# Kernel optimization log

Measured on AMD Instinct MI355X. Metric: run time of the kernel, lower is better.

Reference implementation:

```python
import jax, jax.numpy as jnp
import numpy as np

BLOCK = 128
SPARSE_BLOCK = 128
SF = 4
NEG = jnp.finfo(jnp.float32).min


def _unfold(x, size, step):
    # x: (..., T, d) -> (..., b, size, d) overlapping windows (torch unfold + transpose)
    b = (x.shape[-2] - size) // step + 1
    idx = np.arange(b)[:, None] * step + np.arange(size)
    return x[..., idx, :]


def _pad_tokens(x, s, pad_value):
    cfg = [(0, 0)] * (x.ndim - 2) + [(s, s), (0, 0)]
    return jnp.pad(x, cfg, constant_values=pad_value)


def _local_blocks(x, pad_value):
    size, step = BLOCK * 3, BLOCK
    s = (size - step) // 2
    return _unfold(_pad_tokens(x, s, pad_value), size, step)


def _sparse_blocks(x, pad_value):
    size0, step = SPARSE_BLOCK * 3, BLOCK // SF
    odd = step % 2
    size = size0 * 2
    s = (size - step) // 2 + odd
    xw = _unfold(_pad_tokens(x, s, pad_value), size, step)
    if odd:
        xw = xw[..., :-1, :, :]
    u = (size - BLOCK * 3 // SF) // 2 + odd
    sb = SPARSE_BLOCK
    u_ = u + odd
    return jnp.concatenate([xw[..., u - sb:u, :], xw[..., -u_:-u_ + sb, :]], axis=-2)


def _cat_gsl(x_global, x_sparse, x_local):
    # x_local: (n,h,b,t_loc,d); broadcast global over block axis
    b = x_local.shape[-3]
    g = jnp.broadcast_to(x_global[..., None, :, :],
                         x_global.shape[:-2] + (b,) + x_global.shape[-2:])
    return jnp.concatenate([g, x_sparse, x_local], axis=-2)


def _build_lsg(x, x_sparse, x_global, pad_value):
    loc = _local_blocks(x, pad_value)
    sp = _sparse_blocks(x_sparse, pad_value)
    return _cat_gsl(x_global, sp, loc)


def reference(query_layer, key_layer, value_layer, attention_mask,
              sparse_key, sparse_value, sparse_mask,
              global_key, global_value, global_mask):
    n, h, t, d = query_layer.shape
    n_blocks = t // BLOCK

    keys = _build_lsg(key_layer, sparse_key, global_key, 0.0)      # (n,h,b,K,d)
    vals = _build_lsg(value_layer, sparse_value, global_value, 0.0)

    # masks: (n,1,1,T) treated as d=1 token data after transpose
    m = jnp.swapaxes(attention_mask, -1, -2)    # (n,1,t,1)
    sm = jnp.swapaxes(sparse_mask, -1, -2)      # (n,1,t/SF,1)
    gm = jnp.swapaxes(global_mask, -1, -2)      # (n,1,g,1)
    mask = _build_lsg(m, sm, gm, NEG)           # (n,1,b,K,1)
    mask = jnp.swapaxes(mask, -1, -2)           # (n,1,b,1,K)

    q = query_layer.reshape(n, h, n_blocks, BLOCK, d)
    scores = jnp.einsum('nhbqd,nhbkd->nhbqk', q, keys) / jnp.sqrt(jnp.float32(d))
    probs = jax.nn.softmax(scores + mask, axis=-1)
    ctx = jnp.einsum('nhbqk,nhbkd->nhbqd', probs, vals)
    return ctx.reshape(n, h, t, d)


def setup_inputs() -> dict:
    key = jax.random.key(0)
    n, h, t, d = 2, 12, 4096, 64
    g = 64
    ts = t // SF
    k = jax.random.split(key, 7)
    return {
        'query_layer': jax.random.normal(k[0], (n, h, t, d), jnp.float32),
        'key_layer': jax.random.normal(k[1], (n, h, t, d), jnp.float32),
        'value_layer': jax.random.normal(k[2], (n, h, t, d), jnp.float32),
        'attention_mask': jnp.zeros((n, 1, 1, t), jnp.float32),
        'sparse_key': jax.random.normal(k[3], (n, h, ts, d), jnp.float32),
        'sparse_value': jax.random.normal(k[4], (n, h, ts, d), jnp.float32),
        'sparse_mask': jnp.zeros((n, 1, 1, ts), jnp.float32),
        'global_key': jax.random.normal(k[5], (n, h, g, d), jnp.float32),
        'global_value': jax.random.normal(k[6], (n, h, g, d), jnp.float32),
        'global_mask': jnp.zeros((n, 1, 1, g), jnp.float32),
    }
```

## Files before the change

kernel.cpp:

```cpp
#include <hip/hip_runtime.h>
#include <hip/hip_bf16.h>

typedef __attribute__((ext_vector_type(8))) short short8;
typedef __attribute__((ext_vector_type(4))) float f32x4;

#define LOG2E 1.44269504f
#define SCL2  0.18033688f
#define MNEG  -3.0e38f
#define MINIT -1.0e30f

__device__ __forceinline__ short f2bf(float f) {
  union { float f; unsigned u; } x; x.f = f;
  return (short)((x.u + 0x7FFFu + ((x.u >> 16) & 1u)) >> 16);
}
__device__ __forceinline__ float exp2g(float x) {
  float r; asm("v_exp_f32 %0, %1" : "=v"(r) : "v"(x)); return r;
}
__device__ __forceinline__ unsigned cvt_pk_bf16(float lo, float hi) {
  unsigned r;
  asm("v_cvt_pk_bf16_f32 %0, %1, %2" : "=v"(r) : "v"(lo), "v"(hi));
  return r;
}

__device__ __forceinline__ void conv_one(
    const float* __restrict__ src, short* __restrict__ dst,
    int Tin, int pad, int cid) {
  int Tpad = Tin + 2 * pad;
  int row = cid >> 3;
  int d0 = (cid & 7) * 8;
  int tok = row % Tpad;
  int nh = row / Tpad;
  int st = tok - pad;
  short8 o;
  if (st >= 0 && st < Tin) {
    const float4* sp = (const float4*)(src + ((size_t)nh * Tin + st) * 64 + d0);
    float4 f0 = sp[0], f1 = sp[1];
    o[0] = f2bf(f0.x); o[1] = f2bf(f0.y); o[2] = f2bf(f0.z); o[3] = f2bf(f0.w);
    o[4] = f2bf(f1.x); o[5] = f2bf(f1.y); o[6] = f2bf(f1.z); o[7] = f2bf(f1.w);
  } else {
#pragma unroll
    for (int j = 0; j < 8; ++j) o[j] = 0;
  }
  *(short8*)(dst + (size_t)row * 64 + d0) = o;
}

__global__ __launch_bounds__(256) void conv_fused(
    const float* __restrict__ K, const float* __restrict__ SK,
    const float* __restrict__ GK,
    short* __restrict__ KL, short* __restrict__ KS, short* __restrict__ KG,
    const float* __restrict__ am, const float* __restrict__ sm,
    const float* __restrict__ gm,
    float* __restrict__ AM2, float* __restrict__ SM2, float* __restrict__ GM2) {
  int cid = blockIdx.x * 256 + threadIdx.x;
  const int nL = 24 * 4352 * 8;
  const int nS = nL + 24 * 1344 * 8;
  const int nG = nS + 24 * 64 * 8;
  if (cid < nL) { conv_one(K, KL, 4096, 128, cid); return; }
  if (cid < nS) { conv_one(SK, KS, 1024, 160, cid - nL); return; }
  if (cid < nG) { conv_one(GK, KG, 64, 0, cid - nS); return; }
  int i = cid - nG;
  if (i < 2 * 4352) {
    int n = i / 4352, rr = i % 4352, s = rr - 128;
    AM2[i] = (s >= 0 && s < 4096) ? am[n * 4096 + s] * LOG2E : MNEG;
  } else if (i < 2 * 4352 + 2 * 1344) {
    int j = i - 2 * 4352;
    int n = j / 1344, rr = j % 1344, s = rr - 160;
    SM2[j] = (s >= 0 && s < 1024) ? sm[n * 1024 + s] * LOG2E : MNEG;
  } else if (i < 2 * 4352 + 2 * 1344 + 2 * 64) {
    int j = i - 2 * 4352 - 2 * 1344;
    GM2[j] = gm[j] * LOG2E;
  }
}

__device__ __forceinline__ void transv_one(
    const float* __restrict__ src, short* __restrict__ dst,
    int Tin, int pad, int tiles, int bidx, int tid, short (*lt)[72]) {
  int tile = bidx % tiles;
  int nh = bidx / tiles;
  int Tpad = Tin + 2 * pad;
  int c0 = tile * 64;
  int tok = tid >> 2;
  int dc = (tid & 3) * 16;
  int st = c0 + tok - pad;
  if (st >= 0 && st < Tin) {
    const float4* sp = (const float4*)(src + ((size_t)nh * Tin + st) * 64 + dc);
#pragma unroll
    for (int i = 0; i < 4; ++i) {
      float4 f = sp[i];
      lt[tok][dc + i * 4 + 0] = f2bf(f.x);
      lt[tok][dc + i * 4 + 1] = f2bf(f.y);
      lt[tok][dc + i * 4 + 2] = f2bf(f.z);
      lt[tok][dc + i * 4 + 3] = f2bf(f.w);
    }
  } else {
#pragma unroll
    for (int i = 0; i < 16; ++i) lt[tok][dc + i] = 0;
  }
  __syncthreads();
  int d = tid >> 2;
  int tc = (tid & 3) * 16;
  short8 o0, o1;
#pragma unroll
  for (int j = 0; j < 8; ++j) { o0[j] = lt[tc + j][d]; o1[j] = lt[tc + 8 + j][d]; }
  short* dp = dst + ((size_t)nh * 64 + d) * Tpad + c0 + tc;
  *(short8*)(dp) = o0;
  *(short8*)(dp + 8) = o1;
}

__global__ __launch_bounds__(256) void transv_fused(
    const float* __restrict__ V, const float* __restrict__ SV,
    const float* __restrict__ GV,
    short* __restrict__ VTL, short* __restrict__ VTS, short* __restrict__ VTG) {
  __shared__ short lt[64][72];
  int bidx = blockIdx.x;
  int tid = threadIdx.x;
  if (bidx < 24 * 68) { transv_one(V, VTL, 4096, 128, 68, bidx, tid, lt); return; }
  bidx -= 24 * 68;
  if (bidx < 24 * 21) { transv_one(SV, VTS, 1024, 160, 21, bidx, tid, lt); return; }
  bidx -= 24 * 21;
  transv_one(GV, VTG, 64, 0, 1, bidx, tid, lt);
}

__global__ __launch_bounds__(512, 4) void lsg_attn5(
    const short* __restrict__ KL, const short* __restrict__ VTL,
    const short* __restrict__ KS, const short* __restrict__ VTS,
    const short* __restrict__ KG, const short* __restrict__ VTG,
    const float* __restrict__ AM2, const float* __restrict__ SM2,
    const float* __restrict__ GM2,
    const float* __restrict__ q_, float* __restrict__ out) {
  constexpr int TPL = 4352, TPS = 1344;
  __shared__ __align__(16) char smem[49152];

  int bid = blockIdx.x;
  bid = (bid & 7) * 96 + (bid >> 3);
  const int b = bid & 31, nh = bid >> 5, n_ = nh / 12;
  const int tid = threadIdx.x;
  const int wid = tid >> 6, lane = tid & 63;
  const int c = lane & 15, g = lane >> 4;
  const int r = tid >> 3, ch = tid & 7;
  const int skey = 4 * (r & 15) + (r >> 4);
  char* pbase = smem + 32768 + wid * 2048;
  const unsigned stg = ((unsigned)r << 7) + ((unsigned)(ch * 16) ^ ((unsigned)(r & 7) << 4));

  const float* qb = q_ + ((size_t)nh * 4096 + (size_t)b * 128 + wid * 16) * 64;
  short8 qa[2];
#pragma unroll
  for (int kc = 0; kc < 2; ++kc) {
    const float* qp = qb + (size_t)c * 64 + kc * 32 + g * 8;
    float4 f0 = *(const float4*)(qp);
    float4 f1 = *(const float4*)(qp + 4);
    short8 tq;
    tq[0] = f2bf(f0.x); tq[1] = f2bf(f0.y); tq[2] = f2bf(f0.z); tq[3] = f2bf(f0.w);
    tq[4] = f2bf(f1.x); tq[5] = f2bf(f1.y); tq[6] = f2bf(f1.z); tq[7] = f2bf(f1.w);
    qa[kc] = tq;
  }

  f32x4 acc[4];
  float mrun[4], lrun[4];
#pragma unroll
  for (int dd = 0; dd < 4; ++dd) acc[dd] = f32x4{0.f, 0.f, 0.f, 0.f};
#pragma unroll
  for (int j = 0; j < 4; ++j) { mrun[j] = MINIT; lrun[j] = 0.f; }

  auto src_for = [&](int t, const short*& kp, const short*& vp,
                     const float*& mp, int& stride) {
    if (t == 0) {
      kp = KG + (size_t)nh * (64 * 64);
      vp = VTG + (size_t)nh * (64 * 64);
      mp = GM2 + n_ * 64;
      stride = 64;
    } else if (t <= 4) {
      int r0 = b * 32 + (t - 1) * 64 + (t >= 3 ? 96 : 0);
      kp = KS + ((size_t)nh * TPS + r0) * 64;
      vp = VTS + (size_t)nh * (64 * TPS) + r0;
      mp = SM2 + n_ * TPS + r0;
      stride = TPS;
    } else {
      int r0 = b * 128 + (t - 5) * 64;
      kp = KL + ((size_t)nh * TPL + r0) * 64;
      vp = VTL + (size_t)nh * (64 * TPL) + r0;
      mp = AM2 + n_ * TPL + r0;
      stride = TPL;
    }
  };

  short8 kr, vr;
  float m_cur[4], m_nxt[4];

  {
    const short* kp; const short* vp; const float* mp; int st;
    src_for(0, kp, vp, mp, st);
    kr = *(const short8*)(kp + skey * 64 + ch * 8);
    vr = *(const short8*)(vp + (size_t)r * st + ch * 8);
#pragma unroll
    for (int i = 0; i < 4; ++i) m_cur[i] = mp[4 * c + i];
    *(short8*)(smem + stg) = kr;
    *(short8*)(smem + 16384 + stg) = vr;
    src_for(1, kp, vp, mp, st);
    kr = *(const short8*)(kp + skey * 64 + ch * 8);
    vr = *(const short8*)(vp + (size_t)r * st + ch * 8);
  }

  for (int t = 0; t < 11; ++t) {
    asm volatile("s_waitcnt lgkmcnt(0)\n\ts_barrier" ::: "memory");
    const int cur = t & 1, nxt = cur ^ 1;
    char* kbuf = smem + cur * 8192;
    char* vbuf = smem + 16384 + cur * 8192;

    short8 bk[4][2];
#pragma unroll
    for (int kt = 0; kt < 4; ++kt)
#pragma unroll
      for (int kc = 0; kc < 2; ++kc) {
        unsigned off = ((unsigned)(kt * 16 + c) << 7) +
                       ((unsigned)(kc * 64 + g * 16) ^ ((unsigned)(c & 7) << 4));
        bk[kt][kc] = *(const short8*)(kbuf + off);
      }

    if (t < 10) {
      *(short8*)(smem + nxt * 8192 + stg) = kr;
      *(short8*)(smem + 16384 + nxt * 8192 + stg) = vr;
    }
    if (t < 9) {
      const short* kp; const short* vp; const float* mp; int st;
      src_for(t + 2, kp, vp, mp, st);
      kr = *(const short8*)(kp + skey * 64 + ch * 8);
      vr = *(const short8*)(vp + (size_t)r * st + ch * 8);
    }
    if (t < 10) {
      const short* kp; const short* vp; const float* mp; int st;
      src_for(t + 1, kp, vp, mp, st);
#pragma unroll
      for (int i = 0; i < 4; ++i) m_nxt[i] = mp[4 * c + i];
    }

    f32x4 s4[4];
    __builtin_amdgcn_s_setprio(1);
#pragma unroll
    for (int kt = 0; kt < 4; ++kt) {
      f32x4 z = f32x4{0.f, 0.f, 0.f, 0.f};
      z = __builtin_amdgcn_mfma_f32_16x16x32_bf16(qa[0], bk[kt][0], z, 0, 0, 0);
      z = __builtin_amdgcn_mfma_f32_16x16x32_bf16(qa[1], bk[kt][1], z, 0, 0, 0);
      s4[kt] = z;
    }
    __builtin_amdgcn_s_setprio(0);
#pragma unroll
    for (int kt = 0; kt < 4; ++kt)
#pragma unroll
      for (int j = 0; j < 4; ++j)
        s4[kt][j] = fmaf(s4[kt][j], SCL2, m_cur[kt]);

    float rs[4];
    float worst = 0.f;
#pragma unroll
    for (int j = 0; j < 4; ++j) {
      float mo = mrun[j];
      float p0 = exp2g(s4[0][j] - mo);
      float p1 = exp2g(s4[1][j] - mo);
      float p2 = exp2g(s4[2][j] - mo);
      float p3 = exp2g(s4[3][j] - mo);
      rs[j] = (p0 + p1) + (p2 + p3);
      worst = fmaxf(worst, rs[j]);
      unsigned w0 = cvt_pk_bf16(p0, p1);
      unsigned w1 = cvt_pk_bf16(p2, p3);
      int row = 4 * g + j;
      unsigned bo = ((unsigned)row << 7) + ((unsigned)c << 3);
      bo ^= (unsigned)((row & 7) << 4);
      uint2 u; u.x = w0; u.y = w1;
      *(uint2*)(pbase + bo) = u;
    }

    if (__any(worst > 4096.f)) {
#pragma unroll
      for (int j = 0; j < 4; ++j) {
        float v0 = s4[0][j], v1 = s4[1][j];
        float v2 = s4[2][j], v3 = s4[3][j];
        float tv = fmaxf(fmaxf(v0, v1), fmaxf(v2, v3));
        tv = fmaxf(tv, __shfl_xor(tv, 1));
        tv = fmaxf(tv, __shfl_xor(tv, 2));
        tv = fmaxf(tv, __shfl_xor(tv, 4));
        tv = fmaxf(tv, __shfl_xor(tv, 8));
        float mo = mrun[j];
        float mn = fmaxf(mo, tv);
        float sc = exp2g(mo - mn);
#pragma unroll
        for (int dd = 0; dd < 4; ++dd) acc[dd][j] *= sc;
        float p0 = exp2g(v0 - mn), p1 = exp2g(v1 - mn);
        float p2 = exp2g(v2 - mn), p3 = exp2g(v3 - mn);
        lrun[j] = lrun[j] * sc + ((p0 + p1) + (p2 + p3));
        mrun[j] = mn;
        unsigned w0 = cvt_pk_bf16(p0, p1);
        unsigned w1 = cvt_pk_bf16(p2, p3);
        int row = 4 * g + j;
        unsigned bo = ((unsigned)row << 7) + ((unsigned)c << 3);
        bo ^= (unsigned)((row & 7) << 4);
        uint2 u; u.x = w0; u.y = w1;
        *(uint2*)(pbase + bo) = u;
      }
    } else {
#pragma unroll
      for (int j = 0; j < 4; ++j) lrun[j] += rs[j];
    }

#pragma unroll
    for (int kk = 0; kk < 2; ++kk) {
      unsigned bo = ((unsigned)c << 7) + (unsigned)(kk * 64 + g * 16);
      bo ^= (unsigned)((c & 7) << 4);
      short8 pa = *(const short8*)(pbase + bo);
      __builtin_amdgcn_s_setprio(1);
#pragma unroll
      for (int dd = 0; dd < 4; ++dd) {
        unsigned voff = ((unsigned)(dd * 16 + c) << 7) +
                        ((unsigned)(kk * 64 + g * 16) ^ ((unsigned)(c & 7) << 4));
        short8 bv = *(const short8*)(vbuf + voff);
        acc[dd] = __builtin_amdgcn_mfma_f32_16x16x32_bf16(pa, bv, acc[dd], 0, 0, 0);
      }
      __builtin_amdgcn_s_setprio(0);
    }
#pragma unroll
    for (int i = 0; i < 4; ++i) m_cur[i] = m_nxt[i];
  }

  float inv[4];
#pragma unroll
  for (int j = 0; j < 4; ++j) {
    float l = lrun[j];
    l += __shfl_xor(l, 1);
    l += __shfl_xor(l, 2);
    l += __shfl_xor(l, 4);
    l += __shfl_xor(l, 8);
    inv[j] = 1.f / l;
  }
  __syncthreads();
  float* fst = (float*)smem + wid * (16 * 68);
#pragma unroll
  for (int j = 0; j < 4; ++j)
#pragma unroll
    for (int dd = 0; dd < 4; ++dd)
      fst[(4 * g + j) * 68 + dd * 16 + c] = acc[dd][j] * inv[j];
  int rr = lane >> 2, cc = lane & 3;
  const float* fs = (float*)smem + wid * (16 * 68) + rr * 68 + cc * 16;
  float* op = out + ((size_t)nh * 4096 + (size_t)b * 128 + wid * 16 + rr) * 64 + cc * 16;
#pragma unroll
  for (int i = 0; i < 4; ++i)
    *(float4*)(op + i * 4) = *(const float4*)(fs + i * 4);
}

__global__ __launch_bounds__(256) void lsg_attn_fb(
    const float* __restrict__ q_,  const float* __restrict__ k_,
    const float* __restrict__ v_,  const float* __restrict__ amask,
    const float* __restrict__ sk,  const float* __restrict__ sv,
    const float* __restrict__ smk, const float* __restrict__ gk,
    const float* __restrict__ gv,  const float* __restrict__ gmk,
    float* __restrict__ out) {
  constexpr int T = 4096, D = 64, TS = 1024;
  constexpr float NEGF = -3.402823466e38f;
  __shared__ __align__(16) short k_lds[32][72];
  __shared__ __align__(16) short v_lds[64][40];
  __shared__ __align__(16) short p_lds[4][32][40];
  __shared__ float m_lds[32];
  const int bid = blockIdx.x;
  const int b = bid & 31, nh = bid >> 5, n_ = nh / 12;
  const int tid = threadIdx.x, wid = tid >> 6, lane = tid & 63;
  const int c = lane & 15, g = lane >> 4;
  const float* qb = q_ + ((size_t)nh * T + (size_t)b * 128) * D;
  const float* kb = k_ + (size_t)nh * T * D;
  const float* vb = v_ + (size_t)nh * T * D;
  const float* skb = sk + (size_t)nh * TS * D;
  const float* svb = sv + (size_t)nh * TS * D;
  const float* gkb = gk + (size_t)nh * 64 * D;
  const float* gvb = gv + (size_t)nh * 64 * D;
  const float* am = amask + (size_t)n_ * T;
  const float* sm = smk + (size_t)n_ * TS;
  const float* gm = gmk + (size_t)n_ * 64;
  short8 qa[2][2];
#pragma unroll
  for (int mt = 0; mt < 2; ++mt)
#pragma unroll
    for (int kc = 0; kc < 2; ++kc) {
      const float* qp = qb + (size_t)(wid * 32 + mt * 16 + c) * D + kc * 32 + g * 8;
      short8 t;
#pragma unroll
      for (int j = 0; j < 8; ++j) t[j] = f2bf(qp[j]);
      qa[mt][kc] = t;
    }
  f32x4 acc[2][4];
#pragma unroll
  for (int mt = 0; mt < 2; ++mt)
#pragma unroll
    for (int dd = 0; dd < 4; ++dd) acc[mt][dd] = f32x4{0.f, 0.f, 0.f, 0.f};
  float mrun[2][4], lrun[2][4];
#pragma unroll
  for (int mt = 0; mt < 2; ++mt)
#pragma unroll
    for (int j = 0; j < 4; ++j) { mrun[mt][j] = NEGF; lrun[mt][j] = 0.f; }
  const int key_local = tid >> 3;
  const int seg = tid & 7;
  const int d0 = seg * 8;
  for (int tile = 0; tile < 22; ++tile) {
    __syncthreads();
    {
      const int kk = tile * 32 + key_local;
      const float* ksrc; const float* vsrc; float mval; bool valid;
      if (kk < 64) {
        ksrc = gkb + kk * D; vsrc = gvb + kk * D; mval = gm[kk]; valid = true;
      } else if (kk < 320) {
        int s = b * 32 - 160 + (kk - 64) + ((kk >= 192) ? 96 : 0);
        valid = (s >= 0) && (s < TS);
        int sc2 = valid ? s : 0;
        ksrc = skb + sc2 * D; vsrc = svb + sc2 * D;
        mval = valid ? sm[sc2] : NEGF;
      } else {
        int tt = b * 128 - 128 + (kk - 320);
        valid = (tt >= 0) && (tt < T);
        int tc = valid ? tt : 0;
        ksrc = kb + tc * D; vsrc = vb + tc * D;
        mval = valid ? am[tc] : NEGF;
      }
      short8 k8; short v8[8];
      if (valid) {
#pragma unroll
        for (int j = 0; j < 8; ++j) { k8[j] = f2bf(ksrc[d0 + j]); v8[j] = f2bf(vsrc[d0 + j]); }
      } else {
#pragma unroll
        for (int j = 0; j < 8; ++j) { k8[j] = 0; v8[j] = 0; }
      }
      *(short8*)(&k_lds[key_local][d0]) = k8;
#pragma unroll
      for (int j = 0; j < 8; ++j) v_lds[d0 + j][key_local] = v8[j];
      if (seg == 0) m_lds[key_local] = mval;
    }
    __syncthreads();
    short8 bk[2][2];
#pragma unroll
    for (int kt = 0; kt < 2; ++kt)
#pragma unroll
      for (int kc = 0; kc < 2; ++kc)
        bk[kt][kc] = *(const short8*)(&k_lds[kt * 16 + c][kc * 32 + g * 8]);
    f32x4 s_[2][2];
#pragma unroll
    for (int mt = 0; mt < 2; ++mt)
#pragma unroll
      for (int kt = 0; kt < 2; ++kt) {
        f32x4 z = f32x4{0.f, 0.f, 0.f, 0.f};
        z = __builtin_amdgcn_mfma_f32_16x16x32_bf16(qa[mt][0], bk[kt][0], z, 0, 0, 0);
        z = __builtin_amdgcn_mfma_f32_16x16x32_bf16(qa[mt][1], bk[kt][1], z, 0, 0, 0);
        s_[mt][kt] = z;
      }
    const float msk0 = m_lds[c];
    const float msk1 = m_lds[16 + c];
#pragma unroll
    for (int mt = 0; mt < 2; ++mt) {
#pragma unroll
      for (int j = 0; j < 4; ++j) {
        float s0 = s_[mt][0][j] * 0.125f + msk0;
        float s1 = s_[mt][1][j] * 0.125f + msk1;
        float tv = fmaxf(s0, s1);
        tv = fmaxf(tv, __shfl_xor(tv, 1));
        tv = fmaxf(tv, __shfl_xor(tv, 2));
        tv = fmaxf(tv, __shfl_xor(tv, 4));
        tv = fmaxf(tv, __shfl_xor(tv, 8));
        float mold = mrun[mt][j];
        float mnew = fmaxf(mold, tv);
        float scale = __expf(mold - mnew);
        mrun[mt][j] = mnew;
        float p0 = __expf(s0 - mnew);
        float p1 = __expf(s1 - mnew);
        lrun[mt][j] = lrun[mt][j] * scale + p0 + p1;
#pragma unroll
        for (int dd = 0; dd < 4; ++dd) acc[mt][dd][j] *= scale;
        p_lds[wid][mt * 16 + g * 4 + j][c] = f2bf(p0);
        p_lds[wid][mt * 16 + g * 4 + j][16 + c] = f2bf(p1);
      }
    }
    __syncthreads();
#pragma unroll
    for (int mt = 0; mt < 2; ++mt) {
      short8 pa = *(const short8*)(&p_lds[wid][mt * 16 + c][g * 8]);
#pragma unroll
      for (int dd = 0; dd < 4; ++dd) {
        short8 bv = *(const short8*)(&v_lds[dd * 16 + c][g * 8]);
        acc[mt][dd] = __builtin_amdgcn_mfma_f32_16x16x32_bf16(pa, bv, acc[mt][dd], 0, 0, 0);
      }
    }
  }
  float* ob = out + ((size_t)nh * T + (size_t)b * 128 + (size_t)wid * 32) * D;
#pragma unroll
  for (int mt = 0; mt < 2; ++mt)
#pragma unroll
    for (int j = 0; j < 4; ++j) {
      float l = lrun[mt][j];
      l += __shfl_xor(l, 1);
      l += __shfl_xor(l, 2);
      l += __shfl_xor(l, 4);
      l += __shfl_xor(l, 8);
      float inv = 1.f / l;
      int row = mt * 16 + g * 4 + j;
#pragma unroll
      for (int dd = 0; dd < 4; ++dd)
        ob[(size_t)row * D + dd * 16 + c] = acc[mt][dd][j] * inv;
    }
}

extern "C" void kernel_launch(void* const* d_in, const int* in_sizes, int n_in,
                              void* d_out, int out_size, void* d_ws, size_t ws_size,
                              hipStream_t stream) {
  const float* q  = (const float*)d_in[0];
  const float* k  = (const float*)d_in[1];
  const float* v  = (const float*)d_in[2];
  const float* am = (const float*)d_in[3];
  const float* sk = (const float*)d_in[4];
  const float* sv = (const float*)d_in[5];
  const float* sm = (const float*)d_in[6];
  const float* gk = (const float*)d_in[7];
  const float* gv = (const float*)d_in[8];
  const float* gm = (const float*)d_in[9];
  float* out = (float*)d_out;

  size_t off = 0;
  char* base = (char*)d_ws;
  auto alloc = [&](size_t bytes) { void* p = base + off; off += bytes; return p; };
  short* KL  = (short*)alloc(13369344);
  short* VTL = (short*)alloc(13369344);
  short* KS  = (short*)alloc(4128768);
  short* VTS = (short*)alloc(4128768);
  short* KG  = (short*)alloc(196608);
  short* VTG = (short*)alloc(196608);
  float* AM2 = (float*)alloc(34816);
  float* SM2 = (float*)alloc(10752);
  float* GM2 = (float*)alloc(512);

  if (off <= ws_size) {
    hipLaunchKernelGGL(conv_fused, dim3(4365), dim3(256), 0, stream,
                       k, sk, gk, KL, KS, KG, am, sm, gm, AM2, SM2, GM2);
    hipLaunchKernelGGL(transv_fused, dim3(2160), dim3(256), 0, stream,
                       v, sv, gv, VTL, VTS, VTG);
    hipLaunchKernelGGL(lsg_attn5, dim3(768), dim3(512), 0, stream,
                       KL, VTL, KS, VTS, KG, VTG, AM2, SM2, GM2, q, out);
  } else {
    hipLaunchKernelGGL(lsg_attn_fb, dim3(768), dim3(256), 0, stream,
                       q, k, v, am, sk, sv, sm, gk, gv, gm, out);
  }
}
```

Before: 59.52 us.

## Merge prepass kernels and skip fully padded key tiles per block

The K-conversion, V-transpose and mask prepasses are merged into one launch, which removes one kernel launch and its boundary. The attention kernel now builds a per-block list of key tiles and drops tiles that, for edge blocks, lie entirely in the padding region. Those tiles are fully masked, so edge blocks do less load and MFMA work. The tile index is now a runtime value, which may cost some unrolling and address-computation efficiency, and the merged prepass mixes block types that use shared memory differently.

```diff
diff --git a/kernel.cpp b/kernel.cpp
--- a/kernel.cpp
+++ b/kernel.cpp
@@ -44,34 +44,6 @@
   *(short8*)(dst + (size_t)row * 64 + d0) = o;
 }
 
-__global__ __launch_bounds__(256) void conv_fused(
-    const float* __restrict__ K, const float* __restrict__ SK,
-    const float* __restrict__ GK,
-    short* __restrict__ KL, short* __restrict__ KS, short* __restrict__ KG,
-    const float* __restrict__ am, const float* __restrict__ sm,
-    const float* __restrict__ gm,
-    float* __restrict__ AM2, float* __restrict__ SM2, float* __restrict__ GM2) {
-  int cid = blockIdx.x * 256 + threadIdx.x;
-  const int nL = 24 * 4352 * 8;
-  const int nS = nL + 24 * 1344 * 8;
-  const int nG = nS + 24 * 64 * 8;
-  if (cid < nL) { conv_one(K, KL, 4096, 128, cid); return; }
-  if (cid < nS) { conv_one(SK, KS, 1024, 160, cid - nL); return; }
-  if (cid < nG) { conv_one(GK, KG, 64, 0, cid - nS); return; }
-  int i = cid - nG;
-  if (i < 2 * 4352) {
-    int n = i / 4352, rr = i % 4352, s = rr - 128;
-    AM2[i] = (s >= 0 && s < 4096) ? am[n * 4096 + s] * LOG2E : MNEG;
-  } else if (i < 2 * 4352 + 2 * 1344) {
-    int j = i - 2 * 4352;
-    int n = j / 1344, rr = j % 1344, s = rr - 160;
-    SM2[j] = (s >= 0 && s < 1024) ? sm[n * 1024 + s] * LOG2E : MNEG;
-  } else if (i < 2 * 4352 + 2 * 1344 + 2 * 64) {
-    int j = i - 2 * 4352 - 2 * 1344;
-    GM2[j] = gm[j] * LOG2E;
-  }
-}
-
 __device__ __forceinline__ void transv_one(
     const float* __restrict__ src, short* __restrict__ dst,
     int Tin, int pad, int tiles, int bidx, int tid, short (*lt)[72]) {
@@ -107,21 +79,46 @@
   *(short8*)(dp + 8) = o1;
 }
 
-__global__ __launch_bounds__(256) void transv_fused(
+__global__ __launch_bounds__(256) void prepass_all(
+    const float* __restrict__ K, const float* __restrict__ SK,
+    const float* __restrict__ GK,
     const float* __restrict__ V, const float* __restrict__ SV,
     const float* __restrict__ GV,
-    short* __restrict__ VTL, short* __restrict__ VTS, short* __restrict__ VTG) {
+    short* __restrict__ KL, short* __restrict__ KS, short* __restrict__ KG,
+    short* __restrict__ VTL, short* __restrict__ VTS, short* __restrict__ VTG,
+    const float* __restrict__ am, const float* __restrict__ sm,
+    const float* __restrict__ gm,
+    float* __restrict__ AM2, float* __restrict__ SM2, float* __restrict__ GM2) {
   __shared__ short lt[64][72];
   int bidx = blockIdx.x;
   int tid = threadIdx.x;
-  if (bidx < 24 * 68) { transv_one(V, VTL, 4096, 128, 68, bidx, tid, lt); return; }
-  bidx -= 24 * 68;
-  if (bidx < 24 * 21) { transv_one(SV, VTS, 1024, 160, 21, bidx, tid, lt); return; }
-  bidx -= 24 * 21;
-  transv_one(GV, VTG, 64, 0, 1, bidx, tid, lt);
-}
-
-__global__ __launch_bounds__(512, 4) void lsg_attn5(
+  if (bidx < 3264) { conv_one(K,  KL, 4096, 128, bidx * 256 + tid); return; }
+  bidx -= 3264;
+  if (bidx < 1008) { conv_one(SK, KS, 1024, 160, bidx * 256 + tid); return; }
+  bidx -= 1008;
+  if (bidx < 48)   { conv_one(GK, KG, 64, 0, bidx * 256 + tid); return; }
+  bidx -= 48;
+  if (bidx < 1632) { transv_one(V,  VTL, 4096, 128, 68, bidx, tid, lt); return; }
+  bidx -= 1632;
+  if (bidx < 504)  { transv_one(SV, VTS, 1024, 160, 21, bidx, tid, lt); return; }
+  bidx -= 504;
+  if (bidx < 24)   { transv_one(GV, VTG, 64, 0, 1, bidx, tid, lt); return; }
+  bidx -= 24;
+  int i = bidx * 256 + tid;
+  if (i < 2 * 4352) {
+    int n = i / 4352, rr = i % 4352, s = rr - 128;
+    AM2[i] = (s >= 0 && s < 4096) ? am[n * 4096 + s] * LOG2E : MNEG;
+  } else if (i < 2 * 4352 + 2 * 1344) {
+    int j = i - 2 * 4352;
+    int n = j / 1344, rr = j % 1344, s = rr - 160;
+    SM2[j] = (s >= 0 && s < 1024) ? sm[n * 1024 + s] * LOG2E : MNEG;
+  } else {
+    int j = i - 2 * 4352 - 2 * 1344;
+    GM2[j] = gm[j] * LOG2E;
+  }
+}
+
+__global__ __launch_bounds__(512, 4) void lsg_attn8(
     const short* __restrict__ KL, const short* __restrict__ VTL,
     const short* __restrict__ KS, const short* __restrict__ VTS,
     const short* __restrict__ KG, const short* __restrict__ VTG,
@@ -141,6 +138,19 @@
   const int skey = 4 * (r & 15) + (r >> 4);
   char* pbase = smem + 32768 + wid * 2048;
   const unsigned stg = ((unsigned)r << 7) + ((unsigned)(ch * 16) ^ ((unsigned)(r & 7) << 4));
+
+  unsigned long long enc = 0; int nt = 0;
+  {
+    auto push = [&](int t) { enc |= (unsigned long long)t << (4 * nt); ++nt; };
+    push(0);
+    if (b >= 4)  push(1);
+    if (b >= 2)  push(2);
+    if (b <= 29) push(3);
+    if (b <= 27) push(4);
+    if (b >= 1)  { push(5); push(6); }
+    push(7); push(8);
+    if (b <= 30) { push(9); push(10); }
+  }
 
   const float* qb = q_ + ((size_t)nh * 4096 + (size_t)b * 128 + wid * 16) * 64;
   short8 qa[2];
@@ -196,14 +206,14 @@
     for (int i = 0; i < 4; ++i) m_cur[i] = mp[4 * c + i];
     *(short8*)(smem + stg) = kr;
     *(short8*)(smem + 16384 + stg) = vr;
-    src_for(1, kp, vp, mp, st);
+    src_for((int)((enc >> 4) & 15ull), kp, vp, mp, st);
     kr = *(const short8*)(kp + skey * 64 + ch * 8);
     vr = *(const short8*)(vp + (size_t)r * st + ch * 8);
   }
 
-  for (int t = 0; t < 11; ++t) {
+  for (int i = 0; i < nt; ++i) {
     asm volatile("s_waitcnt lgkmcnt(0)\n\ts_barrier" ::: "memory");
-    const int cur = t & 1, nxt = cur ^ 1;
+    const int cur = i & 1, nxt = cur ^ 1;
     char* kbuf = smem + cur * 8192;
     char* vbuf = smem + 16384 + cur * 8192;
 
@@ -217,21 +227,23 @@
         bk[kt][kc] = *(const short8*)(kbuf + off);
       }
 
-    if (t < 10) {
+    if (i + 1 < nt) {
       *(short8*)(smem + nxt * 8192 + stg) = kr;
       *(short8*)(smem + 16384 + nxt * 8192 + stg) = vr;
     }
-    if (t < 9) {
+    if (i + 2 < nt) {
+      int tn = (int)((enc >> (4 * (i + 2))) & 15ull);
       const short* kp; const short* vp; const float* mp; int st;
-      src_for(t + 2, kp, vp, mp, st);
+      src_for(tn, kp, vp, mp, st);
       kr = *(const short8*)(kp + skey * 64 + ch * 8);
       vr = *(const short8*)(vp + (size_t)r * st + ch * 8);
     }
-    if (t < 10) {
+    if (i + 1 < nt) {
+      int tn = (int)((enc >> (4 * (i + 1))) & 15ull);
       const short* kp; const short* vp; const float* mp; int st;
-      src_for(t + 1, kp, vp, mp, st);
-#pragma unroll
-      for (int i = 0; i < 4; ++i) m_nxt[i] = mp[4 * c + i];
+      src_for(tn, kp, vp, mp, st);
+#pragma unroll
+      for (int j = 0; j < 4; ++j) m_nxt[j] = mp[4 * c + j];
     }
 
     f32x4 s4[4];
@@ -318,7 +330,7 @@
       __builtin_amdgcn_s_setprio(0);
     }
 #pragma unroll
-    for (int i = 0; i < 4; ++i) m_cur[i] = m_nxt[i];
+    for (int j = 0; j < 4; ++j) m_cur[j] = m_nxt[j];
   }
 
   float inv[4];
@@ -531,11 +543,10 @@
   float* GM2 = (float*)alloc(512);
 
   if (off <= ws_size) {
-    hipLaunchKernelGGL(conv_fused, dim3(4365), dim3(256), 0, stream,
-                       k, sk, gk, KL, KS, KG, am, sm, gm, AM2, SM2, GM2);
-    hipLaunchKernelGGL(transv_fused, dim3(2160), dim3(256), 0, stream,
-                       v, sv, gv, VTL, VTS, VTG);
-    hipLaunchKernelGGL(lsg_attn5, dim3(768), dim3(512), 0, stream,
+    hipLaunchKernelGGL(prepass_all, dim3(6525), dim3(256), 0, stream,
+                       k, sk, gk, v, sv, gv, KL, KS, KG, VTL, VTS, VTG,
+                       am, sm, gm, AM2, SM2, GM2);
+    hipLaunchKernelGGL(lsg_attn8, dim3(768), dim3(512), 0, stream,
                        KL, VTL, KS, VTS, KG, VTG, AM2, SM2, GM2, q, out);
   } else {
     hipLaunchKernelGGL(lsg_attn_fb, dim3(768), dim3(256), 0, stream,
```

Result: no change. 58.56 us (-1.6%).
